# Optimization experiments

Hardware: AMD Instinct MI355X
Metric: run time of the kernel (lower is better)

The kernel has to match this reference:

```python
import jax, jax.numpy as jnp
import numpy as np

N = 160000   # active voxels
C = 64       # embed_channels
K = 2048     # clusters per level
G = 128      # voxel grid side (grid_size)
NEG = 0.01   # LeakyReLU negative slope (torch default)
EPS_BN = 1e-5


def _build_neighbors():
    # Random unique active voxels in a G^3 grid; 27-neighborhood index map for SubMConv3d.
    rng = np.random.default_rng(0)
    codes = np.sort(rng.choice(G ** 3, size=N, replace=False))
    xc = codes // (G * G); yc = (codes // G) % G; zc = codes % G
    nbrs = []
    for dx in (-1, 0, 1):
        for dy in (-1, 0, 1):
            for dz in (-1, 0, 1):
                nx, ny, nz = xc + dx, yc + dy, zc + dz
                inb = (nx >= 0) & (nx < G) & (ny >= 0) & (ny < G) & (nz >= 0) & (nz < G)
                ncode = nx * (G * G) + ny * G + nz
                pos = np.searchsorted(codes, np.where(inb, ncode, 0))
                pos = np.clip(pos, 0, N - 1)
                found = inb & (codes[pos] == ncode)
                nbrs.append(np.where(found, pos, -1))
    return np.stack(nbrs).astype(np.int32)  # [27, N], -1 = no active neighbor


def setup_inputs():
    key = jax.random.key(0)
    def nrm(i, shape, s=0.05):
        return jax.random.normal(jax.random.fold_in(key, i), shape, jnp.float32) * s
    return {
        'feat': jax.random.normal(jax.random.fold_in(key, 0), (N, C), jnp.float32),
        'lw_W': nrm(1, (3, C, C)), 'lw_g': jnp.ones((3, C)), 'lw_b': jnp.zeros((3, C)),
        'w_W': nrm(2, (3, C, C)),
        'proj_W': nrm(3, (4, C, C)), 'proj_g': jnp.ones((4, C)), 'proj_b': jnp.zeros((4, C)),
        'adaptive_W': nrm(4, (C, 3)),
        'fuse_W': nrm(5, (2 * C, C)), 'fuse_g': jnp.ones((C,)), 'fuse_b': jnp.zeros((C,)),
        'conv1_W': nrm(6, (27, C, C)), 'bn1_g': jnp.ones((C,)), 'bn1_b': jnp.zeros((C,)),
        'conv2_W': nrm(7, (27, C, C)), 'bn2_g': jnp.ones((C,)), 'bn2_b': jnp.zeros((C,)),
        'clusters': jax.random.randint(jax.random.fold_in(key, 8), (3, N), 0, K, dtype=jnp.int32),
        'nbr': jnp.asarray(_build_neighbors()),
    }


def _bn(x, g, b):
    # BatchNorm1d, training-mode (biased batch stats over N)
    m = x.mean(0)
    v = x.var(0)
    return (x - m) * jax.lax.rsqrt(v + EPS_BN) * g + b


def _lrelu(x):
    return jax.nn.leaky_relu(x, NEG)


def _seg_sum(x, seg):
    return jax.ops.segment_sum(x, seg, num_segments=K)


def _subm_conv(f, nbr, W):
    # Submanifold 3x3x3 conv: per kernel offset, masked gather + [C,C] matmul.
    out = jnp.zeros((f.shape[0], W.shape[-1]), f.dtype)
    for k in range(27):
        idx = nbr[k]
        g = jnp.where((idx >= 0)[:, None], f[jnp.maximum(idx, 0)], 0.0)
        out = out + g @ W[k]
    return out


def reference(feat, lw_W, lw_g, lw_b, w_W, proj_W, proj_g, proj_b, adaptive_W,
              fuse_W, fuse_g, fuse_b, conv1_W, bn1_g, bn1_b, conv2_W, bn2_g, bn2_b,
              clusters, nbr):
    feats = []
    for i in range(3):  # depth-1 cluster levels
        c = clusters[i]
        cnt = jnp.clip(_seg_sum(jnp.ones((feat.shape[0], 1), feat.dtype), c), 1.0, None)
        pw = _lrelu(_bn(feat @ lw_W[i], lw_g[i], lw_b[i]))
        pw = pw - (_seg_sum(pw, c) / cnt)[c]          # center by cluster mean
        pw = pw @ w_W[i]
        pw = jnp.exp(pw - pw.max())                    # global-max-stabilized exp
        pw = pw / (_seg_sum(pw, c)[c] + 1e-6)          # per-cluster softmax
        pfeat = _lrelu(_bn(feat @ proj_W[i], proj_g[i], proj_b[i])) * pw
        feats.append(_seg_sum(pfeat, c)[c])            # pool then broadcast back
    adp = jax.nn.softmax(feat @ adaptive_W, axis=1)    # [N, 3]
    feats = jnp.stack(feats, axis=1)                   # [N, 3, C]
    feats = jnp.einsum('ln,lnc->lc', adp, feats)
    f = _lrelu(_bn(feat @ proj_W[3], proj_g[3], proj_b[3]))
    f = jnp.concatenate([f, feats], axis=1)
    f = _lrelu(_bn(f @ fuse_W, fuse_g, fuse_b)) + feat
    res = f
    v = _lrelu(_bn(_subm_conv(f, nbr, conv1_W), bn1_g, bn1_b))
    v = _bn(_subm_conv(v, nbr, conv2_W), bn2_g, bn2_b)
    return _lrelu(v + res)
```

## Files before the change

kernel.cpp:

```cpp
#include <hip/hip_runtime.h>
#include <hip/hip_bf16.h>
#include <math.h>

#define KCL 2048
#define LRELU_NEG 0.01f
#define EPSBN 1e-5f

using s8v = __attribute__((ext_vector_type(8))) short;
using f4v = __attribute__((ext_vector_type(4))) float;

union U8 { ushort u[8]; uint4 v; };

__device__ __forceinline__ float lrelu(float x) { return x > 0.f ? x : LRELU_NEG * x; }
__device__ __forceinline__ ushort f2bf(float f) {
    __hip_bfloat16 h = __float2bfloat16(f);
    return *reinterpret_cast<ushort*>(&h);
}
__device__ __forceinline__ float bf2f(ushort u) { return __uint_as_float(((unsigned)u) << 16); }

__device__ __forceinline__ unsigned encf(float f) {
    unsigned u = __float_as_uint(f);
    return (u & 0x80000000u) ? ~u : (u | 0x80000000u);
}
__device__ __forceinline__ float decf(unsigned u) {
    return __uint_as_float((u & 0x80000000u) ? (u & 0x7fffffffu) : ~u);
}

__device__ __forceinline__ void bn_sb(const double* __restrict__ stats, const float* __restrict__ g,
                                      const float* __restrict__ b, int n, float* sb) {
    int t = threadIdx.x;
    if (t < 64) {
        float mean = (float)(stats[t] / n);
        float ex2 = (float)(stats[64 + t] / n);
        float var = fmaxf(ex2 - mean * mean, 0.f);
        float rstd = rsqrtf(var + EPSBN);
        float sc = rstd * g[t];
        sb[t] = sc;
        sb[64 + t] = b[t] - mean * sc;
    }
    __syncthreads();
}

__device__ __forceinline__ void mfma_tileG(const uint4* As, const ushort* Wmat, int ws, int koff,
                                           int rowA0, int rowA1, int swA0, int swA1,
                                           int l15, int lg, f4v acc[2][4]) {
    const s8v* Av = (const s8v*)As;
#pragma unroll
    for (int kb = 0; kb < 2; ++kb) {
        int gch = kb * 4 + lg;
        s8v a0 = Av[rowA0 * 8 + (gch ^ swA0)];
        s8v a1 = Av[rowA1 * 8 + (gch ^ swA1)];
#pragma unroll
        for (int nf = 0; nf < 4; ++nf) {
            int col = nf * 16 + l15;
            s8v bf = *(const s8v*)(Wmat + (size_t)col * ws + koff + gch * 8);
            acc[0][nf] = __builtin_amdgcn_mfma_f32_16x16x32_bf16(a0, bf, acc[0][nf], 0, 0, 0);
            acc[1][nf] = __builtin_amdgcn_mfma_f32_16x16x32_bf16(a1, bf, acc[1][nf], 0, 0, 0);
        }
    }
}

__device__ __forceinline__ void stage_a_bf16(const ushort* S, uint4* As, int row, int n, int arow, int ah) {
    uint4 c0 = {0, 0, 0, 0}, c1 = c0, c2 = c0, c3 = c0;
    if (row < n) {
        const uint4* s = (const uint4*)(S + (size_t)row * 64) + ah * 4;
        c0 = s[0]; c1 = s[1]; c2 = s[2]; c3 = s[3];
    }
    int sw = arow & 7;
    uint4* dst = As + arow * 8;
    dst[(ah * 4 + 0) ^ sw] = c0;
    dst[(ah * 4 + 1) ^ sw] = c1;
    dst[(ah * 4 + 2) ^ sw] = c2;
    dst[(ah * 4 + 3) ^ sw] = c3;
}

__device__ __forceinline__ void stage_a_vals(const float* vals, uint4* As, int arow, int ah) {
    int sw = arow & 7;
    uint4* dst = As + arow * 8;
#pragma unroll
    for (int c = 0; c < 4; ++c) {
        U8 u;
#pragma unroll
        for (int e = 0; e < 8; ++e) u.u[e] = f2bf(vals[c * 8 + e]);
        dst[(ah * 4 + c) ^ sw] = u.v;
    }
}

__global__ __launch_bounds__(256) void prep_wt64(const float* __restrict__ lw, const float* __restrict__ wW,
                                                 const float* __restrict__ proj, const float* __restrict__ c1,
                                                 const float* __restrict__ c2, ushort* __restrict__ wt) {
    int bk = blockIdx.x;
    const float* W;
    if (bk < 3) W = lw + (size_t)bk * 4096;
    else if (bk < 6) W = wW + (size_t)(bk - 3) * 4096;
    else if (bk < 10) W = proj + (size_t)(bk - 6) * 4096;
    else if (bk < 37) W = c1 + (size_t)(bk - 10) * 4096;
    else W = c2 + (size_t)(bk - 37) * 4096;
    ushort* o = wt + (size_t)bk * 4096;
    for (int i = threadIdx.x; i < 4096; i += 256) {
        int kk = i >> 6, cc = i & 63;
        o[cc * 64 + kk] = f2bf(W[i]);
    }
}

__global__ __launch_bounds__(256) void prep_fuse(const float* __restrict__ Wf, ushort* __restrict__ o) {
    for (int i = threadIdx.x; i < 8192; i += 256) {
        int kk = i >> 6, cc = i & 63;
        o[cc * 128 + kk] = f2bf(Wf[i]);
    }
}

__global__ __launch_bounds__(256) void adp_cvt_kernel(const float* __restrict__ feat, const float* __restrict__ aW,
                                                      float* __restrict__ adp, ushort* __restrict__ feat16, int n) {
    __shared__ float w[192];
    for (int i = threadIdx.x; i < 192; i += 256) w[i] = aW[i];
    __syncthreads();
    for (long row = (long)blockIdx.x * 256 + threadIdx.x; row < n; row += (long)gridDim.x * 256) {
        const float4* fr = (const float4*)(feat + row * 64);
        ushort4* fo = (ushort4*)(feat16 + row * 64);
        float l0 = 0.f, l1 = 0.f, l2 = 0.f;
#pragma unroll
        for (int q = 0; q < 16; ++q) {
            float4 x = fr[q];
            int k = q * 4;
            l0 += x.x * w[k * 3 + 0] + x.y * w[k * 3 + 3] + x.z * w[k * 3 + 6] + x.w * w[k * 3 + 9];
            l1 += x.x * w[k * 3 + 1] + x.y * w[k * 3 + 4] + x.z * w[k * 3 + 7] + x.w * w[k * 3 + 10];
            l2 += x.x * w[k * 3 + 2] + x.y * w[k * 3 + 5] + x.z * w[k * 3 + 8] + x.w * w[k * 3 + 11];
            ushort4 u;
            u.x = f2bf(x.x); u.y = f2bf(x.y); u.z = f2bf(x.z); u.w = f2bf(x.w);
            fo[q] = u;
        }
        float m = fmaxf(l0, fmaxf(l1, l2));
        float e0 = expf(l0 - m), e1 = expf(l1 - m), e2 = expf(l2 - m);
        float inv = 1.f / (e0 + e1 + e2);
        adp[row * 3 + 0] = e0 * inv;
        adp[row * 3 + 1] = e1 * inv;
        adp[row * 3 + 2] = e2 * inv;
    }
}

__global__ __launch_bounds__(256) void hist3_kernel(const int* __restrict__ clusters, int* __restrict__ cnt,
                                                    int n) {
    __shared__ int h[KCL];
    int l = blockIdx.x % 3;
    int nb = gridDim.x / 3, bi = blockIdx.x / 3;
    for (int i = threadIdx.x; i < KCL; i += 256) h[i] = 0;
    __syncthreads();
    const int* cl = clusters + (size_t)l * n;
    for (long i = (long)bi * 256 + threadIdx.x; i < n; i += (long)nb * 256)
        atomicAdd(&h[cl[i]], 1);
    __syncthreads();
    for (int i = threadIdx.x; i < KCL; i += 256) {
        int v = h[i];
        if (v) atomicAdd(&cnt[l * KCL + i], v);
    }
}

__global__ __launch_bounds__(256) void scan_kernel(const int* __restrict__ cnt, int* __restrict__ off,
                                                   int* __restrict__ cursor, int n) {
    int l = blockIdx.x;
    const int* c = cnt + l * KCL;
    __shared__ int part[256];
    __shared__ int pref[256];
    int t = threadIdx.x;
    int base = t * 8;
    int v[8];
    int s = 0;
#pragma unroll
    for (int j = 0; j < 8; ++j) { v[j] = c[base + j]; s += v[j]; }
    part[t] = s;
    __syncthreads();
    if (t == 0) {
        int acc = 0;
        for (int i = 0; i < 256; ++i) { pref[i] = acc; acc += part[i]; }
    }
    __syncthreads();
    int acc = pref[t] + l * n;
#pragma unroll
    for (int j = 0; j < 8; ++j) {
        off[l * KCL + base + j] = acc;
        cursor[l * KCL + base + j] = acc;
        acc += v[j];
    }
}

__global__ __launch_bounds__(256) void scatter_kernel(const int* __restrict__ clusters, int* __restrict__ cursor,
                                                      int* __restrict__ perm, int n) {
    long n3 = (long)n * 3;
    for (long i = (long)blockIdx.x * 256 + threadIdx.x; i < n3; i += (long)gridDim.x * 256) {
        int l = (i >= n) + (i >= 2 * (long)n);
        int c = clusters[i];
        int pos = atomicAdd(&cursor[l * KCL + c], 1);
        perm[pos] = (int)(i - (long)l * n);
    }
}

__device__ __forceinline__ void mega_one(const uint4* As, float* red, const ushort* Wmat, ushort* out,
                                         double* statp, int n, int rb, int w, int lane, int t) {
    const int l15 = lane & 15, lg = lane >> 4;
    int rowA0 = w * 32 + l15, rowA1 = rowA0 + 16;
    f4v acc[2][4];
#pragma unroll
    for (int rf = 0; rf < 2; ++rf)
#pragma unroll
        for (int nf = 0; nf < 4; ++nf)
#pragma unroll
            for (int q = 0; q < 4; ++q) acc[rf][nf][q] = 0.f;
    mfma_tileG(As, Wmat, 64, 0, rowA0, rowA1, rowA0 & 7, rowA1 & 7, l15, lg, acc);
    int base = rb + w * 32;
#pragma unroll
    for (int rf = 0; rf < 2; ++rf)
#pragma unroll
        for (int nf = 0; nf < 4; ++nf)
#pragma unroll
            for (int q = 0; q < 4; ++q) {
                int r = base + rf * 16 + lg * 4 + q;
                if (r < n) out[(size_t)r * 64 + nf * 16 + l15] = f2bf(acc[rf][nf][q]);
            }
#pragma unroll
    for (int nf = 0; nf < 4; ++nf) {
        float s = 0.f, s2 = 0.f;
#pragma unroll
        for (int rf = 0; rf < 2; ++rf)
#pragma unroll
            for (int q = 0; q < 4; ++q) {
                int r = base + rf * 16 + lg * 4 + q;
                if (r < n) {
                    float v = acc[rf][nf][q];
                    s += v;
                    s2 += v * v;
                }
            }
        s += __shfl_xor(s, 16); s += __shfl_xor(s, 32);
        s2 += __shfl_xor(s2, 16); s2 += __shfl_xor(s2, 32);
        if (lg == 0) {
            red[w * 64 + nf * 16 + l15] = s;
            red[256 + w * 64 + nf * 16 + l15] = s2;
        }
    }
    __syncthreads();
    if (t < 64) {
        float s = red[t] + red[64 + t] + red[128 + t] + red[192 + t];
        float s2 = red[256 + t] + red[320 + t] + red[384 + t] + red[448 + t];
        atomicAdd(&statp[t], (double)s);
        atomicAdd(&statp[64 + t], (double)s2);
    }
    __syncthreads();
}

__global__ __launch_bounds__(256) void mega7_gemm(const ushort* __restrict__ feat16,
                                                  const ushort* __restrict__ wt64,
                                                  ushort* __restrict__ o0, ushort* __restrict__ o1,
                                                  ushort* __restrict__ o2, ushort* __restrict__ o3,
                                                  ushort* __restrict__ o4, ushort* __restrict__ o5,
                                                  ushort* __restrict__ o6,
                                                  int n, double* __restrict__ stats) {
    __shared__ uint4 As[128 * 8];
    __shared__ float red[512];
    int t = threadIdx.x, lane = t & 63, w = t >> 6;
    int rb = blockIdx.x * 128;
    int arow = t >> 1, ah = t & 1;
    stage_a_bf16(feat16, As, rb + arow, n, arow, ah);
    __syncthreads();
    mega_one(As, red, wt64 + (size_t)0 * 4096, o0, stats + 0 * 128, n, rb, w, lane, t);
    mega_one(As, red, wt64 + (size_t)1 * 4096, o1, stats + 2 * 128, n, rb, w, lane, t);
    mega_one(As, red, wt64 + (size_t)2 * 4096, o2, stats + 4 * 128, n, rb, w, lane, t);
    mega_one(As, red, wt64 + (size_t)6 * 4096, o3, stats + 1 * 128, n, rb, w, lane, t);
    mega_one(As, red, wt64 + (size_t)7 * 4096, o4, stats + 3 * 128, n, rb, w, lane, t);
    mega_one(As, red, wt64 + (size_t)8 * 4096, o5, stats + 5 * 128, n, rb, w, lane, t);
    mega_one(As, red, wt64 + (size_t)9 * 4096, o6, stats + 6 * 128, n, rb, w, lane, t);
}

__global__ __launch_bounds__(256) void reduce_mean3_kernel(const ushort* __restrict__ A3,
                                                           const double* __restrict__ stats,
                                                           const float* __restrict__ lw_g,
                                                           const float* __restrict__ lw_b, int n,
                                                           const int* __restrict__ cnts, const int* __restrict__ offs,
                                                           const int* __restrict__ perm,
                                                           float* __restrict__ meanB3) {
    int l = blockIdx.x >> 11, c = blockIdx.x & (KCL - 1);
    const ushort* A = A3 + (size_t)l * n * 64;
    __shared__ float sb[128];
    bn_sb(stats + (size_t)(2 * l) * 128, lw_g + l * 64, lw_b + l * 64, n, sb);
    int t = threadIdx.x, col = t & 63, rg = t >> 6;
    int o = offs[l * KCL + c], m = cnts[l * KCL + c];
    float acc = 0.f;
    float sc = sb[col], bi = sb[64 + col];
    for (int j = rg; j < m; j += 4) {
        int row = perm[o + j];
        acc += lrelu(bf2f(A[(size_t)row * 64 + col]) * sc + bi);
    }
    __shared__ float red[256];
    red[t] = acc;
    __syncthreads();
    if (t < 64) {
        float s = red[t] + red[t + 64] + red[t + 128] + red[t + 192];
        float cf = (float)m;
        if (cf < 1.f) cf = 1.f;
        meanB3[(size_t)l * KCL * 64 + (size_t)c * 64 + col] = s / cf;
    }
}

__global__ __launch_bounds__(256) void mw3_gemm(const float* __restrict__ meanB3, const ushort* __restrict__ wW16,
                                                float* __restrict__ MW3) {
    __shared__ uint4 As[128 * 8];
    int l = blockIdx.x >> 4, b = blockIdx.x & 15;
    const float* src = meanB3 + (size_t)l * KCL * 64;
    float* out = MW3 + (size_t)l * KCL * 64;
    int t = threadIdx.x, lane = t & 63, w = t >> 6;
    int rb = b * 128;
    int arow = t >> 1, ah = t & 1;
    const int l15 = lane & 15, lg = lane >> 4;
    {
        float vals[32];
        const float4* s = (const float4*)(src + (size_t)(rb + arow) * 64 + ah * 32);
#pragma unroll
        for (int q = 0; q < 8; ++q) {
            float4 x = s[q];
            vals[q * 4 + 0] = x.x; vals[q * 4 + 1] = x.y;
            vals[q * 4 + 2] = x.z; vals[q * 4 + 3] = x.w;
        }
        stage_a_vals(vals, As, arow, ah);
    }
    __syncthreads();
    f4v acc[2][4];
#pragma unroll
    for (int rf = 0; rf < 2; ++rf)
#pragma unroll
        for (int nf = 0; nf < 4; ++nf)
#pragma unroll
            for (int q = 0; q < 4; ++q) acc[rf][nf][q] = 0.f;
    int rowA0 = w * 32 + l15, rowA1 = rowA0 + 16;
    mfma_tileG(As, wW16 + (size_t)l * 4096, 64, 0, rowA0, rowA1, rowA0 & 7, rowA1 & 7, l15, lg, acc);
    int base = rb + w * 32;
#pragma unroll
    for (int rf = 0; rf < 2; ++rf)
#pragma unroll
        for (int nf = 0; nf < 4; ++nf)
#pragma unroll
            for (int q = 0; q < 4; ++q) {
                int r = base + rf * 16 + lg * 4 + q;
                out[(size_t)r * 64 + nf * 16 + l15] = acc[rf][nf][q];
            }
}

__global__ __launch_bounds__(256) void cgemm3(ushort* __restrict__ A3io, const ushort* __restrict__ wW16,
                                              const float* __restrict__ MW3, const int* __restrict__ clusters,
                                              const double* __restrict__ stats, const float* __restrict__ lw_g,
                                              const float* __restrict__ lw_b,
                                              unsigned* __restrict__ gmax, int n, int nb) {
    __shared__ uint4 As[128 * 8];
    __shared__ float sb[128];
    int l = blockIdx.x / nb, b = blockIdx.x % nb;
    ushort* A = A3io + (size_t)l * n * 64;
    const float* MW = MW3 + (size_t)l * KCL * 64;
    const int* clus = clusters + (size_t)l * n;
    int t = threadIdx.x, lane = t & 63, w = t >> 6;
    int rb = b * 128;
    int arow = t >> 1, ah = t & 1;
    const int l15 = lane & 15, lg = lane >> 4;

    bn_sb(stats + (size_t)(2 * l) * 128, lw_g + l * 64, lw_b + l * 64, n, sb);
    {
        int row = rb + arow;
        float vals[32];
        if (row < n) {
            const U8* s8p = (const U8*)(A + (size_t)row * 64 + ah * 32);
#pragma unroll
            for (int c = 0; c < 4; ++c) {
                U8 u = s8p[c];
#pragma unroll
                for (int e = 0; e < 8; ++e) {
                    int col = ah * 32 + c * 8 + e;
                    vals[c * 8 + e] = lrelu(bf2f(u.u[e]) * sb[col] + sb[64 + col]);
                }
            }
        } else {
#pragma unroll
            for (int i = 0; i < 32; ++i) vals[i] = 0.f;
        }
        stage_a_vals(vals, As, arow, ah);
    }
    __syncthreads();
    f4v acc[2][4];
#pragma unroll
    for (int rf = 0; rf < 2; ++rf)
#pragma unroll
        for (int nf = 0; nf < 4; ++nf)
#pragma unroll
            for (int q = 0; q < 4; ++q) acc[rf][nf][q] = 0.f;
    int rowA0 = w * 32 + l15, rowA1 = rowA0 + 16;
    mfma_tileG(As, wW16 + (size_t)l * 4096, 64, 0, rowA0, rowA1, rowA0 & 7, rowA1 & 7, l15, lg, acc);
    int base = rb + w * 32;
    float m = -INFINITY;
#pragma unroll
    for (int rf = 0; rf < 2; ++rf)
#pragma unroll
        for (int q = 0; q < 4; ++q) {
            int r = base + rf * 16 + lg * 4 + q;
            if (r < n) {
                int c = clus[r];
                const float* mwr = MW + (size_t)c * 64;
#pragma unroll
                for (int nf = 0; nf < 4; ++nf) {
                    int col = nf * 16 + l15;
                    float v = acc[rf][nf][q] - mwr[col];
                    A[(size_t)r * 64 + col] = f2bf(v);
                    m = fmaxf(m, v);
                }
            }
        }
    __syncthreads();
    float* sp = (float*)As;
    sp[t] = m;
    __syncthreads();
    for (int s = 128; s > 0; s >>= 1) {
        if (t < s) sp[t] = fmaxf(sp[t], sp[t + s]);
        __syncthreads();
    }
    if (t == 0) atomicMax(&gmax[l], encf(sp[0]));
}

__global__ __launch_bounds__(256) void expf3_kernel(const ushort* __restrict__ C3, const ushort* __restrict__ E0,
                                                    const ushort* __restrict__ E1, const ushort* __restrict__ E2,
                                                    const double* __restrict__ stats,
                                                    const float* __restrict__ proj_g, const float* __restrict__ proj_b,
                                                    int n, const unsigned* __restrict__ gmax,
                                                    const int* __restrict__ cnts, const int* __restrict__ offs,
                                                    const int* __restrict__ perm, float* __restrict__ seg3) {
    int l = blockIdx.x >> 11, c = blockIdx.x & (KCL - 1);
    const ushort* C = C3 + (size_t)l * n * 64;
    const ushort* E = (l == 0) ? E0 : (l == 1) ? E1 : E2;
    __shared__ float sb[128];
    bn_sb(stats + (size_t)(2 * l + 1) * 128, proj_g + l * 64, proj_b + l * 64, n, sb);
    int t = threadIdx.x, col = t & 63, rg = t >> 6;
    float gm = decf(gmax[l]);
    int o = offs[l * KCL + c], m = cnts[l * KCL + c];
    float accd = 0.f, accn = 0.f;
    float sc = sb[col], bi = sb[64 + col];
    for (int j = rg; j < m; j += 4) {
        int row = perm[o + j];
        float d = expf(bf2f(C[(size_t)row * 64 + col]) - gm);
        float pf = lrelu(bf2f(E[(size_t)row * 64 + col]) * sc + bi);
        accd += d;
        accn += pf * d;
    }
    __shared__ float redd[256], redn[256];
    redd[t] = accd;
    redn[t] = accn;
    __syncthreads();
    if (t < 64) {
        float sd = redd[t] + redd[t + 64] + redd[t + 128] + redd[t + 192];
        float sn = redn[t] + redn[t + 64] + redn[t + 128] + redn[t + 192];
        seg3[(size_t)l * KCL * 64 + (size_t)c * 64 + col] = sn / (sd + 1e-6f);
    }
}

__global__ __launch_bounds__(256) void fuse_mfma(const ushort* __restrict__ P3, const double* __restrict__ statsP,
                                                 const float* __restrict__ gg, const float* __restrict__ bb, int n,
                                                 const float* __restrict__ adp, const int* __restrict__ clusters,
                                                 const float* __restrict__ s3_0, const float* __restrict__ s3_1,
                                                 const float* __restrict__ s3_2, const ushort* __restrict__ WfT,
                                                 ushort* __restrict__ out, double* __restrict__ stats_out) {
    __shared__ uint4 As[128 * 8];
    __shared__ float sb[128];
    int t = threadIdx.x, lane = t & 63, w = t >> 6;
    int rb = blockIdx.x * 128;
    int arow = t >> 1, ah = t & 1;
    const int l15 = lane & 15, lg = lane >> 4;

    bn_sb(statsP, gg, bb, n, sb);

    f4v acc[2][4];
#pragma unroll
    for (int rf = 0; rf < 2; ++rf)
#pragma unroll
        for (int nf = 0; nf < 4; ++nf)
#pragma unroll
            for (int q = 0; q < 4; ++q) acc[rf][nf][q] = 0.f;

    int rowA0 = w * 32 + l15, rowA1 = rowA0 + 16;
    int row = rb + arow;

    for (int p = 0; p < 2; ++p) {
        if (p) __syncthreads();
        float vals[32];
        if (row < n) {
            if (p == 0) {
                const U8* s8p = (const U8*)(P3 + (size_t)row * 64 + ah * 32);
#pragma unroll
                for (int c = 0; c < 4; ++c) {
                    U8 u = s8p[c];
#pragma unroll
                    for (int e = 0; e < 8; ++e) {
                        int col = ah * 32 + c * 8 + e;
                        vals[c * 8 + e] = lrelu(bf2f(u.u[e]) * sb[col] + sb[64 + col]);
                    }
                }
            } else {
                float a0 = adp[(size_t)row * 3 + 0], a1 = adp[(size_t)row * 3 + 1], a2 = adp[(size_t)row * 3 + 2];
                const float* r0 = s3_0 + (size_t)clusters[row] * 64 + ah * 32;
                const float* r1 = s3_1 + (size_t)clusters[(size_t)n + row] * 64 + ah * 32;
                const float* r2 = s3_2 + (size_t)clusters[2 * (size_t)n + row] * 64 + ah * 32;
#pragma unroll
                for (int i = 0; i < 32; ++i) vals[i] = a0 * r0[i] + a1 * r1[i] + a2 * r2[i];
            }
        } else {
#pragma unroll
            for (int i = 0; i < 32; ++i) vals[i] = 0.f;
        }
        stage_a_vals(vals, As, arow, ah);
        __syncthreads();
        mfma_tileG(As, WfT, 128, p * 64, rowA0, rowA1, rowA0 & 7, rowA1 & 7, l15, lg, acc);
    }
    int base = rb + w * 32;
#pragma unroll
    for (int rf = 0; rf < 2; ++rf)
#pragma unroll
        for (int nf = 0; nf < 4; ++nf)
#pragma unroll
            for (int q = 0; q < 4; ++q) {
                int r = base + rf * 16 + lg * 4 + q;
                if (r < n) out[(size_t)r * 64 + nf * 16 + l15] = f2bf(acc[rf][nf][q]);
            }
    __syncthreads();
    float* sp = (float*)As;
    int gidx = w * 4 + lg;
#pragma unroll
    for (int nf = 0; nf < 4; ++nf) {
        int col = nf * 16 + l15;
        float s = 0.f, s2 = 0.f;
#pragma unroll
        for (int rf = 0; rf < 2; ++rf)
#pragma unroll
            for (int q = 0; q < 4; ++q) {
                int r = base + rf * 16 + lg * 4 + q;
                if (r < n) {
                    float v = acc[rf][nf][q];
                    s += v;
                    s2 += v * v;
                }
            }
        sp[gidx * 64 + col] = s;
        sp[1024 + gidx * 64 + col] = s2;
    }
    __syncthreads();
    if (t < 64) {
        float s = 0.f, s2 = 0.f;
#pragma unroll
        for (int i = 0; i < 16; ++i) {
            s += sp[i * 64 + t];
            s2 += sp[1024 + i * 64 + t];
        }
        atomicAdd(&stats_out[t], (double)s);
        atomicAdd(&stats_out[64 + t], (double)s2);
    }
}

__global__ __launch_bounds__(256) void subm_conv_db(const ushort* __restrict__ fin, const int* __restrict__ nbr,
                                                    const ushort* __restrict__ Wt, ushort* __restrict__ vout,
                                                    int n, double* __restrict__ stats_out) {
    __shared__ uint4 As[2][128 * 8];
    __shared__ uint4 Ws[2][64 * 8];
    int t = threadIdx.x;
    int lane = t & 63, w = t >> 6;
    int rb = blockIdx.x * 128;
    int arow = t >> 1, ah = t & 1;
    int wrow = t >> 2, wq = t & 3;
    const int l15 = lane & 15, lg = lane >> 4;
    int rowA0 = w * 32 + l15, rowA1 = rowA0 + 16;
    int swA0 = rowA0 & 7, swA1 = rowA1 & 7;
    const bool rowok = (rb + arow) < n;
    const int swa = arow & 7, sww = wrow & 7;

    f4v acc[2][4];
#pragma unroll
    for (int rf = 0; rf < 2; ++rf)
#pragma unroll
        for (int nf = 0; nf < 4; ++nf)
#pragma unroll
            for (int q = 0; q < 4; ++q) acc[rf][nf][q] = 0.f;

    bool fc0, fc1, wzc, wzn = false;
    {
        int gi = rowok ? nbr[rb + arow] : -1;
        uint4 v0 = {0, 0, 0, 0}, v1 = v0, v2 = v0, v3 = v0;
        if (gi >= 0) {
            const uint4* src = (const uint4*)(fin + (size_t)gi * 64) + ah * 4;
            v0 = src[0]; v1 = src[1]; v2 = src[2]; v3 = src[3];
        }
        unsigned long long bal = __ballot(gi >= 0);
        fc0 = (bal & 0xffffffffull) != 0ull;
        fc1 = (bal >> 32) != 0ull;
        wzc = (gi < 0);
        uint4* dst = As[0] + arow * 8;
        dst[(ah * 4 + 0) ^ swa] = v0;
        dst[(ah * 4 + 1) ^ swa] = v1;
        dst[(ah * 4 + 2) ^ swa] = v2;
        dst[(ah * 4 + 3) ^ swa] = v3;
        const uint4* ws = (const uint4*)(Wt + (size_t)wrow * 64);
        uint4* wdst = Ws[0] + wrow * 8;
        wdst[wq ^ sww] = ws[wq];
        wdst[(wq + 4) ^ sww] = ws[wq + 4];
    }
    int gi_next = rowok ? nbr[(size_t)n + rb + arow] : -1;
    int cur = 0;

    for (int k = 0; k < 27; ++k) {
        uint4 a0, a1, a2, a3, w0, w1;
        bool fn0 = false, fn1 = false, missn = true;
        if (k < 26) {
            missn = (gi_next < 0);
            a0 = a1 = a2 = a3 = (uint4){0, 0, 0, 0};
            if (!missn) {
                const uint4* src = (const uint4*)(fin + (size_t)gi_next * 64) + ah * 4;
                a0 = src[0]; a1 = src[1]; a2 = src[2]; a3 = src[3];
            }
            unsigned long long bal = __ballot(!missn);
            fn0 = (bal & 0xffffffffull) != 0ull;
            fn1 = (bal >> 32) != 0ull;
            const uint4* ws = (const uint4*)(Wt + (size_t)(k + 1) * 4096 + (size_t)wrow * 64);
            w0 = ws[wq];
            w1 = ws[wq + 4];
            if (k < 25) gi_next = rowok ? nbr[(size_t)(k + 2) * n + rb + arow] : -1;
        }
        __syncthreads();
        if (fc0 | fc1) {
            const s8v* Av = (const s8v*)As[cur];
            const s8v* Wv = (const s8v*)Ws[cur];
#pragma unroll
            for (int kb = 0; kb < 2; ++kb) {
                int gch = kb * 4 + lg;
                s8v bfr[4];
#pragma unroll
                for (int nf = 0; nf < 4; ++nf) {
                    int col = nf * 16 + l15;
                    bfr[nf] = Wv[col * 8 + (gch ^ (col & 7))];
                }
                if (fc0) {
                    s8v av0 = Av[rowA0 * 8 + (gch ^ swA0)];
#pragma unroll
                    for (int nf = 0; nf < 4; ++nf)
                        acc[0][nf] = __builtin_amdgcn_mfma_f32_16x16x32_bf16(av0, bfr[nf], acc[0][nf], 0, 0, 0);
                }
                if (fc1) {
                    s8v av1 = Av[rowA1 * 8 + (gch ^ swA1)];
#pragma unroll
                    for (int nf = 0; nf < 4; ++nf)
                        acc[1][nf] = __builtin_amdgcn_mfma_f32_16x16x32_bf16(av1, bfr[nf], acc[1][nf], 0, 0, 0);
                }
            }
        }
        if (k < 26) {
            if (!(missn && wzn)) {
                uint4* dst = As[cur ^ 1] + arow * 8;
                dst[(ah * 4 + 0) ^ swa] = a0;
                dst[(ah * 4 + 1) ^ swa] = a1;
                dst[(ah * 4 + 2) ^ swa] = a2;
                dst[(ah * 4 + 3) ^ swa] = a3;
            }
            uint4* wdst = Ws[cur ^ 1] + wrow * 8;
            wdst[wq ^ sww] = w0;
            wdst[(wq + 4) ^ sww] = w1;
            cur ^= 1;
            bool nw = wzc;
            wzc = missn;
            wzn = nw;
            fc0 = fn0;
            fc1 = fn1;
        }
    }
    int base = rb + w * 32;
#pragma unroll
    for (int rf = 0; rf < 2; ++rf)
#pragma unroll
        for (int nf = 0; nf < 4; ++nf)
#pragma unroll
            for (int q = 0; q < 4; ++q) {
                int r = base + rf * 16 + lg * 4 + q;
                if (r < n) vout[(size_t)r * 64 + nf * 16 + l15] = f2bf(acc[rf][nf][q]);
            }
    __syncthreads();
    float* sp = (float*)As[0];
    int gidx = w * 4 + lg;
#pragma unroll
    for (int nf = 0; nf < 4; ++nf) {
        int col = nf * 16 + l15;
        float s = 0.f, s2 = 0.f;
#pragma unroll
        for (int rf = 0; rf < 2; ++rf)
#pragma unroll
            for (int q = 0; q < 4; ++q) {
                int r = base + rf * 16 + lg * 4 + q;
                if (r < n) {
                    float v = acc[rf][nf][q];
                    s += v;
                    s2 += v * v;
                }
            }
        sp[gidx * 64 + col] = s;
        sp[1024 + gidx * 64 + col] = s2;
    }
    __syncthreads();
    if (t < 64) {
        float s = 0.f, s2 = 0.f;
#pragma unroll
        for (int i = 0; i < 16; ++i) {
            s += sp[i * 64 + t];
            s2 += sp[1024 + i * 64 + t];
        }
        atomicAdd(&stats_out[t], (double)s);
        atomicAdd(&stats_out[64 + t], (double)s2);
    }
}

__global__ __launch_bounds__(256) void addfeat_kernel(const ushort* __restrict__ t3, const double* __restrict__ stats,
                                                      const float* __restrict__ g, const float* __restrict__ b,
                                                      const float* __restrict__ feat, ushort* __restrict__ f16,
                                                      int n) {
    __shared__ float sb[128];
    bn_sb(stats, g, b, n, sb);
    long total4 = (long)n * 16;
    for (long i = (long)blockIdx.x * 256 + threadIdx.x; i < total4; i += (long)gridDim.x * 256) {
        int c0 = (int)(i & 15) * 4;
        ushort4 xv = ((const ushort4*)t3)[i];
        float4 fz = ((const float4*)feat)[i];
        ushort4 u;
        u.x = f2bf(lrelu(bf2f(xv.x) * sb[c0 + 0] + sb[64 + c0 + 0]) + fz.x);
        u.y = f2bf(lrelu(bf2f(xv.y) * sb[c0 + 1] + sb[64 + c0 + 1]) + fz.y);
        u.z = f2bf(lrelu(bf2f(xv.z) * sb[c0 + 2] + sb[64 + c0 + 2]) + fz.z);
        u.w = f2bf(lrelu(bf2f(xv.w) * sb[c0 + 3] + sb[64 + c0 + 3]) + fz.w);
        ((ushort4*)f16)[i] = u;
    }
}

__global__ __launch_bounds__(256) void bnlrelu_tobf16_kernel(const ushort* __restrict__ v,
                                                             const double* __restrict__ stats,
                                                             const float* __restrict__ g, const float* __restrict__ b,
                                                             ushort* __restrict__ o16, int n) {
    __shared__ float sb[128];
    bn_sb(stats, g, b, n, sb);
    long total4 = (long)n * 16;
    for (long i = (long)blockIdx.x * 256 + threadIdx.x; i < total4; i += (long)gridDim.x * 256) {
        int c0 = (int)(i & 15) * 4;
        ushort4 xv = ((const ushort4*)v)[i];
        ushort4 u;
        u.x = f2bf(lrelu(bf2f(xv.x) * sb[c0 + 0] + sb[64 + c0 + 0]));
        u.y = f2bf(lrelu(bf2f(xv.y) * sb[c0 + 1] + sb[64 + c0 + 1]));
        u.z = f2bf(lrelu(bf2f(xv.z) * sb[c0 + 2] + sb[64 + c0 + 2]));
        u.w = f2bf(lrelu(bf2f(xv.w) * sb[c0 + 3] + sb[64 + c0 + 3]));
        ((ushort4*)o16)[i] = u;
    }
}

__global__ __launch_bounds__(256) void final_kernel(const ushort* __restrict__ w16, const double* __restrict__ stats,
                                                    const float* __restrict__ g, const float* __restrict__ b,
                                                    const ushort* __restrict__ f16, float* __restrict__ out, int n) {
    __shared__ float sb[128];
    bn_sb(stats, g, b, n, sb);
    long total4 = (long)n * 16;
    for (long i = (long)blockIdx.x * 256 + threadIdx.x; i < total4; i += (long)gridDim.x * 256) {
        int c0 = (int)(i & 15) * 4;
        ushort4 xv = ((const ushort4*)w16)[i];
        ushort4 u = ((const ushort4*)f16)[i];
        float4 y;
        y.x = lrelu(bf2f(xv.x) * sb[c0 + 0] + sb[64 + c0 + 0] + bf2f(u.x));
        y.y = lrelu(bf2f(xv.y) * sb[c0 + 1] + sb[64 + c0 + 1] + bf2f(u.y));
        y.z = lrelu(bf2f(xv.z) * sb[c0 + 2] + sb[64 + c0 + 2] + bf2f(u.z));
        y.w = lrelu(bf2f(xv.w) * sb[c0 + 3] + sb[64 + c0 + 3] + bf2f(u.w));
        ((float4*)out)[i] = y;
    }
}

extern "C" void kernel_launch(void* const* d_in, const int* in_sizes, int n_in,
                              void* d_out, int out_size, void* d_ws, size_t ws_size,
                              hipStream_t stream) {
    const float* feat = (const float*)d_in[0];
    const float* lw_W = (const float*)d_in[1];
    const float* lw_g = (const float*)d_in[2];
    const float* lw_b = (const float*)d_in[3];
    const float* w_W = (const float*)d_in[4];
    const float* proj_W = (const float*)d_in[5];
    const float* proj_g = (const float*)d_in[6];
    const float* proj_b = (const float*)d_in[7];
    const float* adaptive_W = (const float*)d_in[8];
    const float* fuse_W = (const float*)d_in[9];
    const float* fuse_g = (const float*)d_in[10];
    const float* fuse_b = (const float*)d_in[11];
    const float* conv1_W = (const float*)d_in[12];
    const float* bn1_g = (const float*)d_in[13];
    const float* bn1_b = (const float*)d_in[14];
    const float* conv2_W = (const float*)d_in[15];
    const float* bn2_g = (const float*)d_in[16];
    const float* bn2_b = (const float*)d_in[17];
    const int* clusters = (const int*)d_in[18];
    const int* nbr = (const int*)d_in[19];

    const int n = in_sizes[0] / 64;

    char* ws = (char*)d_ws;
    size_t off = 0;
    auto alloc = [&](size_t bytes) -> size_t {
        size_t o = off;
        off = (off + bytes + 255) & ~(size_t)255;
        return o;
    };
    size_t cnt_off = alloc((size_t)3 * KCL * 4);
    size_t stats_off = alloc((size_t)10 * 128 * 8);
    size_t gmax_off = alloc(16);
    size_t zbytes = off;
    size_t offs_off = alloc((size_t)3 * KCL * 4);
    size_t cur_off = alloc((size_t)3 * KCL * 4);
    size_t perm_off = alloc((size_t)3 * n * 4);
    size_t mean_off = alloc((size_t)3 * KCL * 64 * 4);
    size_t mw_off = alloc((size_t)3 * KCL * 64 * 4);
    size_t seg3_off = alloc((size_t)3 * KCL * 64 * 4);
    size_t adp_off = alloc((size_t)n * 3 * 4);
    size_t feat16_off = alloc((size_t)n * 64 * 2);
    size_t ra_off = alloc((size_t)3 * n * 64 * 2);
    size_t re_off = alloc((size_t)2 * n * 64 * 2);
    size_t wt64_off = alloc((size_t)64 * 4096 * 2);
    size_t wfT_off = alloc((size_t)8192 * 2);

    int* cnts = (int*)(ws + cnt_off);
    double* stats = (double*)(ws + stats_off);
    unsigned* gmax = (unsigned*)(ws + gmax_off);
    int* offs = (int*)(ws + offs_off);
    int* cursor = (int*)(ws + cur_off);
    int* perm = (int*)(ws + perm_off);
    float* meanB3 = (float*)(ws + mean_off);
    float* MW3 = (float*)(ws + mw_off);
    float* seg3 = (float*)(ws + seg3_off);
    float* adp = (float*)(ws + adp_off);
    ushort* feat16 = (ushort*)(ws + feat16_off);
    ushort* RA = (ushort*)(ws + ra_off);
    ushort* RE = (ushort*)(ws + re_off);
    ushort* wt64 = (ushort*)(ws + wt64_off);
    ushort* wfT = (ushort*)(ws + wfT_off);
    float* outp = (float*)d_out;

    ushort* A3 = RA;
    ushort* E0 = RE;
    ushort* E1 = RE + (size_t)n * 64;
    ushort* E2 = (ushort*)d_out;
    ushort* P3 = (ushort*)d_out + (size_t)n * 64;
    ushort* t3buf = RA;
    ushort* fbuf16 = RA + (size_t)n * 64;
    ushort* c1out = RA + (size_t)2 * n * 64;
    ushort* cbuf = RE;
    ushort* c2out = RE + (size_t)n * 64;

    const ushort* wW16 = wt64 + (size_t)3 * 4096;
    const ushort* conv1W16 = wt64 + (size_t)10 * 4096;
    const ushort* conv2W16 = wt64 + (size_t)37 * 4096;

    hipMemsetAsync(d_ws, 0, zbytes, stream);

    const int GEMM_BLK = (n + 127) / 128;
    const int EW_BLK = 2048;

    prep_wt64<<<64, 256, 0, stream>>>(lw_W, w_W, proj_W, conv1_W, conv2_W, wt64);
    prep_fuse<<<1, 256, 0, stream>>>(fuse_W, wfT);
    adp_cvt_kernel<<<1024, 256, 0, stream>>>(feat, adaptive_W, adp, feat16, n);

    hist3_kernel<<<384, 256, 0, stream>>>(clusters, cnts, n);
    scan_kernel<<<3, 256, 0, stream>>>(cnts, offs, cursor, n);
    scatter_kernel<<<1024, 256, 0, stream>>>(clusters, cursor, perm, n);

    mega7_gemm<<<GEMM_BLK, 256, 0, stream>>>(feat16, wt64,
                                             A3, A3 + (size_t)n * 64, A3 + (size_t)2 * n * 64,
                                             E0, E1, E2, P3, n, stats);
    reduce_mean3_kernel<<<3 * KCL, 256, 0, stream>>>(A3, stats, lw_g, lw_b, n, cnts, offs, perm, meanB3);
    mw3_gemm<<<3 * 16, 256, 0, stream>>>(meanB3, wW16, MW3);
    cgemm3<<<3 * GEMM_BLK, 256, 0, stream>>>(A3, wW16, MW3, clusters, stats, lw_g, lw_b, gmax, n, GEMM_BLK);
    expf3_kernel<<<3 * KCL, 256, 0, stream>>>(A3, E0, E1, E2, stats, proj_g, proj_b, n, gmax,
                                              cnts, offs, perm, seg3);

    fuse_mfma<<<GEMM_BLK, 256, 0, stream>>>(P3, stats + 6 * 128, proj_g + 192, proj_b + 192, n,
                                            adp, clusters,
                                            seg3, seg3 + (size_t)KCL * 64, seg3 + (size_t)2 * KCL * 64,
                                            wfT, t3buf, stats + 7 * 128);
    addfeat_kernel<<<EW_BLK, 256, 0, stream>>>(t3buf, stats + 7 * 128, fuse_g, fuse_b, feat, fbuf16, n);

    subm_conv_db<<<GEMM_BLK, 256, 0, stream>>>(fbuf16, nbr, conv1W16, c1out, n, stats + 8 * 128);
    bnlrelu_tobf16_kernel<<<EW_BLK, 256, 0, stream>>>(c1out, stats + 8 * 128, bn1_g, bn1_b, cbuf, n);

    subm_conv_db<<<GEMM_BLK, 256, 0, stream>>>(cbuf, nbr, conv2W16, c2out, n, stats + 9 * 128);
    final_kernel<<<EW_BLK, 256, 0, stream>>>(c2out, stats + 9 * 128, bn2_g, bn2_b, fbuf16, outp, n);
}
```

Before: 581.7 us.

## Recompute per-level projection GEMM inside segment kernel instead of storing it

```diff
diff --git a/kernel.cpp b/kernel.cpp
--- a/kernel.cpp
+++ b/kernel.cpp
@@ -64,6 +64,20 @@
     uint4 c0 = {0, 0, 0, 0}, c1 = c0, c2 = c0, c3 = c0;
     if (row < n) {
         const uint4* s = (const uint4*)(S + (size_t)row * 64) + ah * 4;
+        c0 = s[0]; c1 = s[1]; c2 = s[2]; c3 = s[3];
+    }
+    int sw = arow & 7;
+    uint4* dst = As + arow * 8;
+    dst[(ah * 4 + 0) ^ sw] = c0;
+    dst[(ah * 4 + 1) ^ sw] = c1;
+    dst[(ah * 4 + 2) ^ sw] = c2;
+    dst[(ah * 4 + 3) ^ sw] = c3;
+}
+
+__device__ __forceinline__ void stage_a_gather(const ushort* S, uint4* As, int gi, int arow, int ah) {
+    uint4 c0 = {0, 0, 0, 0}, c1 = c0, c2 = c0, c3 = c0;
+    if (gi >= 0) {
+        const uint4* s = (const uint4*)(S + (size_t)gi * 64) + ah * 4;
         c0 = s[0]; c1 = s[1]; c2 = s[2]; c3 = s[3];
     }
     int sw = arow & 7;
@@ -195,6 +209,7 @@
     }
 }
 
+template <int WR>
 __device__ __forceinline__ void mega_one(const uint4* As, float* red, const ushort* Wmat, ushort* out,
                                          double* statp, int n, int rb, int w, int lane, int t) {
     const int l15 = lane & 15, lg = lane >> 4;
@@ -208,15 +223,17 @@
             for (int q = 0; q < 4; ++q) acc[rf][nf][q] = 0.f;
     mfma_tileG(As, Wmat, 64, 0, rowA0, rowA1, rowA0 & 7, rowA1 & 7, l15, lg, acc);
     int base = rb + w * 32;
-#pragma unroll
-    for (int rf = 0; rf < 2; ++rf)
-#pragma unroll
-        for (int nf = 0; nf < 4; ++nf)
-#pragma unroll
-            for (int q = 0; q < 4; ++q) {
-                int r = base + rf * 16 + lg * 4 + q;
-                if (r < n) out[(size_t)r * 64 + nf * 16 + l15] = f2bf(acc[rf][nf][q]);
-            }
+    if (WR) {
+#pragma unroll
+        for (int rf = 0; rf < 2; ++rf)
+#pragma unroll
+            for (int nf = 0; nf < 4; ++nf)
+#pragma unroll
+                for (int q = 0; q < 4; ++q) {
+                    int r = base + rf * 16 + lg * 4 + q;
+                    if (r < n) out[(size_t)r * 64 + nf * 16 + l15] = f2bf(acc[rf][nf][q]);
+                }
+    }
 #pragma unroll
     for (int nf = 0; nf < 4; ++nf) {
         float s = 0.f, s2 = 0.f;
@@ -251,9 +268,7 @@
 __global__ __launch_bounds__(256) void mega7_gemm(const ushort* __restrict__ feat16,
                                                   const ushort* __restrict__ wt64,
                                                   ushort* __restrict__ o0, ushort* __restrict__ o1,
-                                                  ushort* __restrict__ o2, ushort* __restrict__ o3,
-                                                  ushort* __restrict__ o4, ushort* __restrict__ o5,
-                                                  ushort* __restrict__ o6,
+                                                  ushort* __restrict__ o2, ushort* __restrict__ o6,
                                                   int n, double* __restrict__ stats) {
     __shared__ uint4 As[128 * 8];
     __shared__ float red[512];
@@ -262,13 +277,13 @@
     int arow = t >> 1, ah = t & 1;
     stage_a_bf16(feat16, As, rb + arow, n, arow, ah);
     __syncthreads();
-    mega_one(As, red, wt64 + (size_t)0 * 4096, o0, stats + 0 * 128, n, rb, w, lane, t);
-    mega_one(As, red, wt64 + (size_t)1 * 4096, o1, stats + 2 * 128, n, rb, w, lane, t);
-    mega_one(As, red, wt64 + (size_t)2 * 4096, o2, stats + 4 * 128, n, rb, w, lane, t);
-    mega_one(As, red, wt64 + (size_t)6 * 4096, o3, stats + 1 * 128, n, rb, w, lane, t);
-    mega_one(As, red, wt64 + (size_t)7 * 4096, o4, stats + 3 * 128, n, rb, w, lane, t);
-    mega_one(As, red, wt64 + (size_t)8 * 4096, o5, stats + 5 * 128, n, rb, w, lane, t);
-    mega_one(As, red, wt64 + (size_t)9 * 4096, o6, stats + 6 * 128, n, rb, w, lane, t);
+    mega_one<1>(As, red, wt64 + (size_t)0 * 4096, o0, stats + 0 * 128, n, rb, w, lane, t);
+    mega_one<1>(As, red, wt64 + (size_t)1 * 4096, o1, stats + 2 * 128, n, rb, w, lane, t);
+    mega_one<1>(As, red, wt64 + (size_t)2 * 4096, o2, stats + 4 * 128, n, rb, w, lane, t);
+    mega_one<0>(As, red, wt64 + (size_t)6 * 4096, nullptr, stats + 1 * 128, n, rb, w, lane, t);
+    mega_one<0>(As, red, wt64 + (size_t)7 * 4096, nullptr, stats + 3 * 128, n, rb, w, lane, t);
+    mega_one<0>(As, red, wt64 + (size_t)8 * 4096, nullptr, stats + 5 * 128, n, rb, w, lane, t);
+    mega_one<1>(As, red, wt64 + (size_t)9 * 4096, o6, stats + 6 * 128, n, rb, w, lane, t);
 }
 
 __global__ __launch_bounds__(256) void reduce_mean3_kernel(const ushort* __restrict__ A3,
@@ -421,38 +436,80 @@
     if (t == 0) atomicMax(&gmax[l], encf(sp[0]));
 }
 
-__global__ __launch_bounds__(256) void expf3_kernel(const ushort* __restrict__ C3, const ushort* __restrict__ E0,
-                                                    const ushort* __restrict__ E1, const ushort* __restrict__ E2,
+__global__ __launch_bounds__(256) void seg3g_kernel(const ushort* __restrict__ C3,
+                                                    const ushort* __restrict__ feat16,
+                                                    const ushort* __restrict__ wt64,
                                                     const double* __restrict__ stats,
-                                                    const float* __restrict__ proj_g, const float* __restrict__ proj_b,
+                                                    const float* __restrict__ proj_g,
+                                                    const float* __restrict__ proj_b,
                                                     int n, const unsigned* __restrict__ gmax,
                                                     const int* __restrict__ cnts, const int* __restrict__ offs,
                                                     const int* __restrict__ perm, float* __restrict__ seg3) {
     int l = blockIdx.x >> 11, c = blockIdx.x & (KCL - 1);
+    __shared__ float sbE[128];
+    __shared__ uint4 As[128 * 8];
+    __shared__ int permL[128];
+    __shared__ float redd[256], redn[256];
+    bn_sb(stats + (size_t)(2 * l + 1) * 128, proj_g + l * 64, proj_b + l * 64, n, sbE);
+    int t = threadIdx.x, lane = t & 63, w = t >> 6;
+    int arow = t >> 1, ah = t & 1;
+    const int l15 = lane & 15, lg = lane >> 4;
+    int rowA0 = w * 32 + l15, rowA1 = rowA0 + 16;
     const ushort* C = C3 + (size_t)l * n * 64;
-    const ushort* E = (l == 0) ? E0 : (l == 1) ? E1 : E2;
-    __shared__ float sb[128];
-    bn_sb(stats + (size_t)(2 * l + 1) * 128, proj_g + l * 64, proj_b + l * 64, n, sb);
-    int t = threadIdx.x, col = t & 63, rg = t >> 6;
+    const ushort* WmP = wt64 + (size_t)(6 + l) * 4096;
     float gm = decf(gmax[l]);
     int o = offs[l * KCL + c], m = cnts[l * KCL + c];
-    float accd = 0.f, accn = 0.f;
-    float sc = sb[col], bi = sb[64 + col];
-    for (int j = rg; j < m; j += 4) {
-        int row = perm[o + j];
-        float d = expf(bf2f(C[(size_t)row * 64 + col]) - gm);
-        float pf = lrelu(bf2f(E[(size_t)row * 64 + col]) * sc + bi);
-        accd += d;
-        accn += pf * d;
-    }
-    __shared__ float redd[256], redn[256];
-    redd[t] = accd;
-    redn[t] = accn;
+    float accd[4] = {0.f, 0.f, 0.f, 0.f}, accn[4] = {0.f, 0.f, 0.f, 0.f};
+
+    for (int ch = 0; ch < m; ch += 128) {
+        int j = ch + arow;
+        int gi = (j < m) ? perm[o + j] : -1;
+        __syncthreads();
+        stage_a_gather(feat16, As, gi, arow, ah);
+        if (ah == 0) permL[arow] = gi;
+        __syncthreads();
+        f4v accE[2][4];
+#pragma unroll
+        for (int rf = 0; rf < 2; ++rf)
+#pragma unroll
+            for (int nf = 0; nf < 4; ++nf)
+#pragma unroll
+                for (int q = 0; q < 4; ++q) accE[rf][nf][q] = 0.f;
+        mfma_tileG(As, WmP, 64, 0, rowA0, rowA1, rowA0 & 7, rowA1 & 7, l15, lg, accE);
+#pragma unroll
+        for (int rf = 0; rf < 2; ++rf)
+#pragma unroll
+            for (int q = 0; q < 4; ++q) {
+                int jl = w * 32 + rf * 16 + lg * 4 + q;
+                if (ch + jl < m) {
+                    int row = permL[jl];
+                    const ushort* Crow = C + (size_t)row * 64;
+#pragma unroll
+                    for (int nf = 0; nf < 4; ++nf) {
+                        int col = nf * 16 + l15;
+                        float d = expf(bf2f(Crow[col]) - gm);
+                        float pf = lrelu(accE[rf][nf][q] * sbE[col] + sbE[64 + col]);
+                        accd[nf] += d;
+                        accn[nf] += pf * d;
+                    }
+                }
+            }
+    }
+#pragma unroll
+    for (int nf = 0; nf < 4; ++nf) {
+        float s = accd[nf], s2 = accn[nf];
+        s += __shfl_xor(s, 16); s += __shfl_xor(s, 32);
+        s2 += __shfl_xor(s2, 16); s2 += __shfl_xor(s2, 32);
+        if (lg == 0) {
+            redd[w * 64 + nf * 16 + l15] = s;
+            redn[w * 64 + nf * 16 + l15] = s2;
+        }
+    }
     __syncthreads();
     if (t < 64) {
-        float sd = redd[t] + redd[t + 64] + redd[t + 128] + redd[t + 192];
-        float sn = redn[t] + redn[t + 64] + redn[t + 128] + redn[t + 192];
-        seg3[(size_t)l * KCL * 64 + (size_t)c * 64 + col] = sn / (sd + 1e-6f);
+        float sd = redd[t] + redd[64 + t] + redd[128 + t] + redd[192 + t];
+        float sn = redn[t] + redn[64 + t] + redn[128 + t] + redn[192 + t];
+        seg3[((size_t)l * KCL + c) * 64 + t] = sn / (sd + 1e-6f);
     }
 }
 
@@ -840,9 +897,6 @@
     float* outp = (float*)d_out;
 
     ushort* A3 = RA;
-    ushort* E0 = RE;
-    ushort* E1 = RE + (size_t)n * 64;
-    ushort* E2 = (ushort*)d_out;
     ushort* P3 = (ushort*)d_out + (size_t)n * 64;
     ushort* t3buf = RA;
     ushort* fbuf16 = RA + (size_t)n * 64;
@@ -869,11 +923,11 @@
 
     mega7_gemm<<<GEMM_BLK, 256, 0, stream>>>(feat16, wt64,
                                              A3, A3 + (size_t)n * 64, A3 + (size_t)2 * n * 64,
-                                             E0, E1, E2, P3, n, stats);
+                                             P3, n, stats);
     reduce_mean3_kernel<<<3 * KCL, 256, 0, stream>>>(A3, stats, lw_g, lw_b, n, cnts, offs, perm, meanB3);
     mw3_gemm<<<3 * 16, 256, 0, stream>>>(meanB3, wW16, MW3);
     cgemm3<<<3 * GEMM_BLK, 256, 0, stream>>>(A3, wW16, MW3, clusters, stats, lw_g, lw_b, gmax, n, GEMM_BLK);
-    expf3_kernel<<<3 * KCL, 256, 0, stream>>>(A3, E0, E1, E2, stats, proj_g, proj_b, n, gmax,
+    seg3g_kernel<<<3 * KCL, 256, 0, stream>>>(A3, feat16, wt64, stats, proj_g, proj_b, n, gmax,
                                               cnts, offs, perm, seg3);
 
     fuse_mfma<<<GEMM_BLK, 256, 0, stream>>>(P3, stats + 6 * 128, proj_g + 192, proj_b + 192, n,
```

After: 589.2 us. Within noise of the previous version (+1.3%).
